# Performance work log

Hardware: AMD Instinct MI355X
Metric: run time of the kernel (lower is better)

Reference implementation:

```python
import jax, jax.numpy as jnp
import numpy as np

B, T, E, V, U = 4096, 80, 100, 10000, 1024


def setup_inputs() -> dict:
    key = jax.random.key(0)
    ks = jax.random.split(key, 8)
    def w(k, shape, fan_in):
        return jax.random.normal(k, shape, jnp.float32) * (1.0 / np.sqrt(fan_in))
    return {
        "inputs": jax.random.randint(ks[0], (B, T), 0, V, dtype=jnp.int32),
        "emb_table": w(ks[1], (V, E), E),
        "Wx0": w(ks[2], (E, U), E),
        "Wh0": w(ks[3], (U, U), U),
        "b0": jnp.zeros((U,), jnp.float32),
        "Wx1": w(ks[4], (U, U), U),
        "Wh1": w(ks[5], (U, U), U),
        "b1": jnp.zeros((U,), jnp.float32),
        "Wfc": w(ks[6], (U, 1), U),
        "bfc": jnp.zeros((1,), jnp.float32),
    }


def reference(inputs, emb_table, Wx0, Wh0, b0, Wx1, Wh1, b1, Wfc, bfc):
    # Embedding lookup: [B, T, E]
    x = emb_table[inputs]
    # Time-major for scan: [T, B, E]
    xs = jnp.swapaxes(x, 0, 1)
    h0_init = jnp.zeros((inputs.shape[0], Wh0.shape[0]), x.dtype)
    h1_init = jnp.zeros((inputs.shape[0], Wh1.shape[0]), x.dtype)

    def step(carry, xt):
        h0, h1 = carry
        # SimpleRNNCell: h' = tanh(x @ Wx + h @ Wh + b); output == new state
        h0 = jnp.tanh(xt @ Wx0 + h0 @ Wh0 + b0)
        h1 = jnp.tanh(h0 @ Wx1 + h1 @ Wh1 + b1)
        return (h0, h1), None

    (h0, h1), _ = jax.lax.scan(step, (h0_init, h1_init), xs)
    # Final dense + sigmoid on last layer-1 output
    prob = jax.nn.sigmoid(h1 @ Wfc + bfc)
    return prob
```

## Files before the change

kernel.cpp:

```cpp
#include <hip/hip_runtime.h>
#include <stdint.h>

#define B_ 4096
#define T_ 80
#define E_ 100
#define V_ 10000
#define U_ 1024

typedef unsigned short u16;
typedef __attribute__((ext_vector_type(8))) __bf16 bf16x8;
typedef __attribute__((ext_vector_type(4))) float f32x4;

__device__ __forceinline__ float bf2f(u16 u) {
    union { unsigned int i; float f; } v; v.i = ((unsigned int)u) << 16; return v.f;
}
__device__ __forceinline__ u16 f2bf(float f) {
    union { float f; unsigned int i; } v; v.f = f;
    unsigned int x = v.i;
    return (u16)((x + 0x7fffu + ((x >> 16) & 1u)) >> 16);
}

__device__ __forceinline__ void load16(const void* g, void* l) {
    __builtin_amdgcn_global_load_lds(
        (__attribute__((address_space(1))) void*)(uintptr_t)g,
        (__attribute__((address_space(3))) void*)(uint32_t)(uintptr_t)l,
        16, 0, 0);
}

__global__ void transpose_pad(const float* __restrict__ src, u16* __restrict__ dst,
                              int K, int N, int Kp)
{
    __shared__ u16 tile[32][33];
    const int k0 = blockIdx.x * 32;
    const int n0 = blockIdx.y * 32;
    const int tx = threadIdx.x & 31;
    const int ty = threadIdx.x >> 5;
#pragma unroll
    for (int i = 0; i < 4; i++) {
        int k = k0 + ty + i * 8;
        tile[ty + i * 8][tx] = (k < K) ? f2bf(src[(size_t)k * N + (n0 + tx)]) : (u16)0;
    }
    __syncthreads();
#pragma unroll
    for (int i = 0; i < 4; i++) {
        int n = n0 + ty + i * 8;
        dst[(size_t)n * Kp + (k0 + tx)] = tile[tx][ty + i * 8];
    }
}

__global__ void embed_pad(const float* __restrict__ emb, u16* __restrict__ dst)
{
    int id = blockIdx.x * 256 + threadIdx.x;
    int v = id >> 7, k = id & 127;
    dst[id] = (k < E_) ? f2bf(emb[v * E_ + k]) : (u16)0;
}

__global__ void __launch_bounds__(256, 2)
rnn_phase(const u16* __restrict__ embP, const int* __restrict__ idx,
          const u16* __restrict__ Wx0T, const u16* __restrict__ Wh0T, const float* __restrict__ b0,
          const u16* __restrict__ Wx1T, const u16* __restrict__ Wh1T, const float* __restrict__ b1,
          const u16* __restrict__ h0r, u16* __restrict__ h0w,
          const u16* __restrict__ h1r, u16* __restrict__ h1w,
          int do0, int do1)
{
    const int linear = blockIdx.x;
    const int layer  = linear >> 8;
    if (layer ? !do1 : !do0) return;

    __shared__ u16 As[2][128 * 64];
    __shared__ u16 Bs[2][128 * 64];
    const int tid  = threadIdx.x;
    const int lane = tid & 63;
    const int wave = tid >> 6;
    const int wm = wave >> 1, wn = wave & 1;
    const int sub = linear & 255;
    const int m0 = (sub & 31) * 128;
    const int n0 = (sub >> 5) * 128;

    const u16 *A1, *W1, *A2, *W2; const float* bias; u16* C; int K1; bool gather;
    if (layer == 0) { A1 = embP; W1 = Wx0T; K1 = 128;  gather = true;  A2 = h0r; W2 = Wh0T; bias = b0; C = h0w; }
    else            { A1 = h0r;  W1 = Wx1T; K1 = 1024; gather = false; A2 = h1r; W2 = Wh1T; bias = b1; C = h1w; }
    const int KB1 = K1 >> 6;
    const int TOT = KB1 + (U_ >> 6);

    const int r8 = lane >> 3;
    const int c8 = lane & 7;

    int gv[4];
    if (gather) {
#pragma unroll
        for (int cc = 0; cc < 4; cc++)
            gv[cc] = idx[(size_t)(m0 + wave * 32 + cc * 8 + r8) * T_];
    }

    const f32x4 z = {0.f, 0.f, 0.f, 0.f};
    f32x4 acc[4][4];
#pragma unroll
    for (int i = 0; i < 4; i++)
#pragma unroll
        for (int j = 0; j < 4; j++) acc[i][j] = z;

    const int l15 = lane & 15, q = lane >> 4, l7 = lane & 7;
    int offA[2][4], offB[2][4];
#pragma unroll
    for (int kk = 0; kk < 2; kk++) {
#pragma unroll
        for (int f = 0; f < 4; f++) {
            const int rA = wm * 64 + f * 16 + l15;
            const int rB = wn * 64 + f * 16 + l15;
            offA[kk][f] = rA * 64 + (((kk * 4 + q) ^ l7) * 8);
            offB[kk][f] = rB * 64 + (((kk * 4 + q) ^ l7) * 8);
        }
    }

    auto stage = [&](int u, int p) {
        u16* Ad = As[p] + wave * 2048;
        u16* Bd = Bs[p] + wave * 2048;
        if (u < KB1) {
            const int k0 = u * 64;
#pragma unroll
            for (int cc = 0; cc < 4; cc++) {
                const int row = wave * 32 + cc * 8 + r8;
                const int scw = (c8 ^ (row & 7)) * 8;
                const u16* ap = gather ? A1 + (size_t)gv[cc] * 128 + k0 + scw
                                       : A1 + (size_t)(m0 + row) * K1 + k0 + scw;
                load16(ap, Ad + cc * 512);
                load16(W1 + (size_t)(n0 + row) * K1 + k0 + scw, Bd + cc * 512);
            }
        } else {
            const int k0 = (u - KB1) * 64;
#pragma unroll
            for (int cc = 0; cc < 4; cc++) {
                const int row = wave * 32 + cc * 8 + r8;
                const int scw = (c8 ^ (row & 7)) * 8;
                load16(A2 + (size_t)(m0 + row) * U_ + k0 + scw, Ad + cc * 512);
                load16(W2 + (size_t)(n0 + row) * U_ + k0 + scw, Bd + cc * 512);
            }
        }
    };

    stage(0, 0);

#pragma unroll 1
    for (int u = 0; u < TOT; ++u) {
        const int p = u & 1;
        __syncthreads();
        if (u + 1 < TOT) stage(u + 1, p ^ 1);
#pragma unroll
        for (int kk = 0; kk < 2; kk++) {
            bf16x8 a[4], b[4];
#pragma unroll
            for (int f = 0; f < 4; f++) {
                a[f] = *reinterpret_cast<const bf16x8*>(As[p] + offA[kk][f]);
                b[f] = *reinterpret_cast<const bf16x8*>(Bs[p] + offB[kk][f]);
            }
#pragma unroll
            for (int i = 0; i < 4; i++)
#pragma unroll
                for (int j = 0; j < 4; j++)
                    acc[i][j] = __builtin_amdgcn_mfma_f32_16x16x32_bf16(a[i], b[j], acc[i][j], 0, 0, 0);
        }
    }

#pragma unroll
    for (int j = 0; j < 4; j++) {
        const int col = n0 + wn * 64 + j * 16 + l15;
        const float bv = bias[col];
#pragma unroll
        for (int i = 0; i < 4; i++) {
#pragma unroll
            for (int r = 0; r < 4; r++) {
                const int row = m0 + wm * 64 + i * 16 + (q << 2) + r;
                float x = acc[i][j][r] + bv;
                x = fminf(15.f, fmaxf(-15.f, x));
                float e = __expf(2.f * x);
                C[(size_t)row * U_ + col] = f2bf((e - 1.f) / (e + 1.f));
            }
        }
    }
}

__global__ void final_dense(const u16* __restrict__ h1, const float* __restrict__ Wfc,
                            const float* __restrict__ bfc, float* __restrict__ out)
{
    const int lane = threadIdx.x & 63;
    const int wave = threadIdx.x >> 6;
    const int row = blockIdx.x * 4 + wave;
    const u16* hp = h1 + (size_t)row * U_ + lane * 16;
    const float* wp = Wfc + lane * 16;
    float s = 0.f;
#pragma unroll
    for (int i = 0; i < 16; i++) s += bf2f(hp[i]) * wp[i];
#pragma unroll
    for (int off = 32; off; off >>= 1) s += __shfl_down(s, off);
    if (lane == 0) {
        float x = s + bfc[0];
        out[row] = 1.f / (1.f + __expf(-x));
    }
}

extern "C" void kernel_launch(void* const* d_in, const int* in_sizes, int n_in,
                              void* d_out, int out_size, void* d_ws, size_t ws_size,
                              hipStream_t stream)
{
    const int*   inputs = (const int*)d_in[0];
    const float* emb    = (const float*)d_in[1];
    const float* Wx0    = (const float*)d_in[2];
    const float* Wh0    = (const float*)d_in[3];
    const float* b0     = (const float*)d_in[4];
    const float* Wx1    = (const float*)d_in[5];
    const float* Wh1    = (const float*)d_in[6];
    const float* b1     = (const float*)d_in[7];
    const float* Wfc    = (const float*)d_in[8];
    const float* bfc    = (const float*)d_in[9];

    char* ws = (char*)d_ws;
    const size_t MB = 1 << 20;
    u16* h0b[2] = { (u16*)(ws + 0 * MB), (u16*)(ws + 8 * MB) };
    u16* h1b[2] = { (u16*)(ws + 16 * MB), (u16*)(ws + 24 * MB) };
    u16* embP = (u16*)(ws + 32 * MB);
    u16* Wx0T = (u16*)(ws + 35 * MB);
    u16* Wh0T = (u16*)(ws + 36 * MB);
    u16* Wx1T = (u16*)(ws + 38 * MB);
    u16* Wh1T = (u16*)(ws + 40 * MB);

    hipMemsetAsync(h0b[1], 0, 8 * MB, stream);
    hipMemsetAsync(h1b[1], 0, 8 * MB, stream);

    embed_pad<<<V_ * 128 / 256, 256, 0, stream>>>(emb, embP);
    transpose_pad<<<dim3(128 / 32, U_ / 32), 256, 0, stream>>>(Wx0, Wx0T, E_, U_, 128);
    transpose_pad<<<dim3(U_ / 32, U_ / 32), 256, 0, stream>>>(Wh0, Wh0T, U_, U_, U_);
    transpose_pad<<<dim3(U_ / 32, U_ / 32), 256, 0, stream>>>(Wx1, Wx1T, U_, U_, U_);
    transpose_pad<<<dim3(U_ / 32, U_ / 32), 256, 0, stream>>>(Wh1, Wh1T, U_, U_, U_);

    for (int p = 0; p <= T_; ++p) {
        const int e = p & 1;
        rnn_phase<<<512, 256, 0, stream>>>(embP, inputs + p,
                                           Wx0T, Wh0T, b0, Wx1T, Wh1T, b1,
                                           h0b[e ^ 1], h0b[e], h1b[e], h1b[e ^ 1],
                                           (int)(p < T_), (int)(p >= 1));
    }
    final_dense<<<B_ / 4, 256, 0, stream>>>(h1b[1], Wfc, bfc, (float*)d_out);
}
```

Measured before the change: 2.762 ms.

## Split layer-1 GEMM into separate input and recurrent roles across phases

Layer 1's two GEMMs are split across pipeline phases. One role computes h0·Wx1 into an fp32 staging buffer. A later role computes h1·Wh1, adds the staged product and applies tanh. This gives three equal-sized roles of 768 blocks per launch instead of one layer-0 role of 18 k-blocks and one layer-1 role of 32 k-blocks, aiming to cut the long-block critical path. The cost is one extra launch, 1.5 waves of blocks per phase, and a 16 MB fp32 write and read per step.

```diff
diff --git a/kernel.cpp b/kernel.cpp
--- a/kernel.cpp
+++ b/kernel.cpp
@@ -61,11 +61,12 @@
           const u16* __restrict__ Wx1T, const u16* __restrict__ Wh1T, const float* __restrict__ b1,
           const u16* __restrict__ h0r, u16* __restrict__ h0w,
           const u16* __restrict__ h1r, u16* __restrict__ h1w,
-          int do0, int do1)
+          const float* __restrict__ x1r, float* __restrict__ x1w,
+          int do0, int doX, int do1)
 {
     const int linear = blockIdx.x;
-    const int layer  = linear >> 8;
-    if (layer ? !do1 : !do0) return;
+    const int role   = linear >> 8;
+    if ((role == 0 && !do0) || (role == 1 && !doX) || (role == 2 && !do1)) return;
 
     __shared__ u16 As[2][128 * 64];
     __shared__ u16 Bs[2][128 * 64];
@@ -77,9 +78,11 @@
     const int m0 = (sub & 31) * 128;
     const int n0 = (sub >> 5) * 128;
 
-    const u16 *A1, *W1, *A2, *W2; const float* bias; u16* C; int K1; bool gather;
-    if (layer == 0) { A1 = embP; W1 = Wx0T; K1 = 128;  gather = true;  A2 = h0r; W2 = Wh0T; bias = b0; C = h0w; }
-    else            { A1 = h0r;  W1 = Wx1T; K1 = 1024; gather = false; A2 = h1r; W2 = Wh1T; bias = b1; C = h1w; }
+    const u16 *A1 = nullptr, *W1 = nullptr, *A2, *W2;
+    int K1 = 0; bool gather = false;
+    if (role == 0)      { A1 = embP; W1 = Wx0T; K1 = 128; gather = true; A2 = h0r; W2 = Wh0T; }
+    else if (role == 1) { A2 = h0r; W2 = Wx1T; }
+    else                { A2 = h1r; W2 = Wh1T; }
     const int KB1 = K1 >> 6;
     const int TOT = KB1 + (U_ >> 6);
 
@@ -162,19 +165,37 @@
         }
     }
 
-#pragma unroll
-    for (int j = 0; j < 4; j++) {
-        const int col = n0 + wn * 64 + j * 16 + l15;
-        const float bv = bias[col];
-#pragma unroll
-        for (int i = 0; i < 4; i++) {
-#pragma unroll
-            for (int r = 0; r < 4; r++) {
-                const int row = m0 + wm * 64 + i * 16 + (q << 2) + r;
-                float x = acc[i][j][r] + bv;
-                x = fminf(15.f, fmaxf(-15.f, x));
-                float e = __expf(2.f * x);
-                C[(size_t)row * U_ + col] = f2bf((e - 1.f) / (e + 1.f));
+    if (role == 1) {
+#pragma unroll
+        for (int j = 0; j < 4; j++) {
+            const int col = n0 + wn * 64 + j * 16 + l15;
+#pragma unroll
+            for (int i = 0; i < 4; i++) {
+#pragma unroll
+                for (int r = 0; r < 4; r++) {
+                    const int row = m0 + wm * 64 + i * 16 + (q << 2) + r;
+                    x1w[(size_t)row * U_ + col] = acc[i][j][r];
+                }
+            }
+        }
+    } else {
+        const float* bias = (role == 0) ? b0 : b1;
+        u16* C = (role == 0) ? h0w : h1w;
+#pragma unroll
+        for (int j = 0; j < 4; j++) {
+            const int col = n0 + wn * 64 + j * 16 + l15;
+            const float bv = bias[col];
+#pragma unroll
+            for (int i = 0; i < 4; i++) {
+#pragma unroll
+                for (int r = 0; r < 4; r++) {
+                    const int row = m0 + wm * 64 + i * 16 + (q << 2) + r;
+                    float x = acc[i][j][r] + bv;
+                    if (role == 2) x += x1r[(size_t)row * U_ + col];
+                    x = fminf(15.f, fmaxf(-15.f, x));
+                    float e = __expf(2.f * x);
+                    C[(size_t)row * U_ + col] = f2bf((e - 1.f) / (e + 1.f));
+                }
             }
         }
     }
@@ -216,13 +237,14 @@
 
     char* ws = (char*)d_ws;
     const size_t MB = 1 << 20;
-    u16* h0b[2] = { (u16*)(ws + 0 * MB), (u16*)(ws + 8 * MB) };
-    u16* h1b[2] = { (u16*)(ws + 16 * MB), (u16*)(ws + 24 * MB) };
-    u16* embP = (u16*)(ws + 32 * MB);
-    u16* Wx0T = (u16*)(ws + 35 * MB);
-    u16* Wh0T = (u16*)(ws + 36 * MB);
-    u16* Wx1T = (u16*)(ws + 38 * MB);
-    u16* Wh1T = (u16*)(ws + 40 * MB);
+    u16*   h0b[2] = { (u16*)(ws + 0 * MB), (u16*)(ws + 8 * MB) };
+    u16*   h1b[2] = { (u16*)(ws + 16 * MB), (u16*)(ws + 24 * MB) };
+    u16*   embP = (u16*)(ws + 32 * MB);
+    u16*   Wx0T = (u16*)(ws + 35 * MB);
+    u16*   Wh0T = (u16*)(ws + 36 * MB);
+    u16*   Wx1T = (u16*)(ws + 38 * MB);
+    u16*   Wh1T = (u16*)(ws + 40 * MB);
+    float* x1b[2] = { (float*)(ws + 48 * MB), (float*)(ws + 64 * MB) };
 
     hipMemsetAsync(h0b[1], 0, 8 * MB, stream);
     hipMemsetAsync(h1b[1], 0, 8 * MB, stream);
@@ -233,12 +255,13 @@
     transpose_pad<<<dim3(U_ / 32, U_ / 32), 256, 0, stream>>>(Wx1, Wx1T, U_, U_, U_);
     transpose_pad<<<dim3(U_ / 32, U_ / 32), 256, 0, stream>>>(Wh1, Wh1T, U_, U_, U_);
 
-    for (int p = 0; p <= T_; ++p) {
-        const int e = p & 1;
-        rnn_phase<<<512, 256, 0, stream>>>(embP, inputs + p,
+    for (int d = 0; d <= T_ + 1; ++d) {
+        const int e = d & 1;
+        rnn_phase<<<768, 256, 0, stream>>>(embP, inputs + d,
                                            Wx0T, Wh0T, b0, Wx1T, Wh1T, b1,
-                                           h0b[e ^ 1], h0b[e], h1b[e], h1b[e ^ 1],
-                                           (int)(p < T_), (int)(p >= 1));
+                                           h0b[e ^ 1], h0b[e], h1b[e ^ 1], h1b[e],
+                                           x1b[e ^ 1], x1b[e],
+                                           (int)(d < T_), (int)(d >= 1 && d <= T_), (int)(d >= 2));
     }
     final_dense<<<B_ / 4, 256, 0, stream>>>(h1b[1], Wfc, bfc, (float*)d_out);
 }
```

Result: slower. 3.960 ms (+43.4%).

## Load B weight fragments directly into registers, bypassing LDS, with a register double buffer

Applied to the files above, without the earlier changes.

Weight (B) tiles are no longer staged through shared memory. Each wave reads its MFMA B fragments straight from global memory into registers, double-buffered across iterations, while A still goes through LDS. The main loop is unrolled by two to alternate between the LDS buffers and the register buffers. This removes LDS traffic and LDS space for B. In exchange, the two waves that share a column block both fetch the same weight data, the global reads are strided and less coalesced, and more VGPRs are needed.

```diff
diff --git a/kernel.cpp b/kernel.cpp
--- a/kernel.cpp
+++ b/kernel.cpp
@@ -68,7 +68,6 @@
     if (layer ? !do1 : !do0) return;
 
     __shared__ u16 As[2][128 * 64];
-    __shared__ u16 Bs[2][128 * 64];
     const int tid  = threadIdx.x;
     const int lane = tid & 63;
     const int wave = tid >> 6;
@@ -101,21 +100,28 @@
         for (int j = 0; j < 4; j++) acc[i][j] = z;
 
     const int l15 = lane & 15, q = lane >> 4, l7 = lane & 7;
-    int offA[2][4], offB[2][4];
+
+    int offA[2][4];
 #pragma unroll
     for (int kk = 0; kk < 2; kk++) {
 #pragma unroll
         for (int f = 0; f < 4; f++) {
             const int rA = wm * 64 + f * 16 + l15;
-            const int rB = wn * 64 + f * 16 + l15;
             offA[kk][f] = rA * 64 + (((kk * 4 + q) ^ l7) * 8);
-            offB[kk][f] = rB * 64 + (((kk * 4 + q) ^ l7) * 8);
-        }
-    }
-
-    auto stage = [&](int u, int p) {
+        }
+    }
+
+    const u16* pB1[4];
+    const u16* pB2[4];
+#pragma unroll
+    for (int f = 0; f < 4; f++) {
+        const int rowB = n0 + wn * 64 + f * 16 + l15;
+        pB1[f] = W1 + (size_t)rowB * K1 + q * 8;
+        pB2[f] = W2 + (size_t)rowB * U_ + q * 8;
+    }
+
+    auto stageA = [&](int u, int p) {
         u16* Ad = As[p] + wave * 2048;
-        u16* Bd = Bs[p] + wave * 2048;
         if (u < KB1) {
             const int k0 = u * 64;
 #pragma unroll
@@ -125,7 +131,6 @@
                 const u16* ap = gather ? A1 + (size_t)gv[cc] * 128 + k0 + scw
                                        : A1 + (size_t)(m0 + row) * K1 + k0 + scw;
                 load16(ap, Ad + cc * 512);
-                load16(W1 + (size_t)(n0 + row) * K1 + k0 + scw, Bd + cc * 512);
             }
         } else {
             const int k0 = (u - KB1) * 64;
@@ -134,32 +139,56 @@
                 const int row = wave * 32 + cc * 8 + r8;
                 const int scw = (c8 ^ (row & 7)) * 8;
                 load16(A2 + (size_t)(m0 + row) * U_ + k0 + scw, Ad + cc * 512);
-                load16(W2 + (size_t)(n0 + row) * U_ + k0 + scw, Bd + cc * 512);
             }
         }
     };
 
-    stage(0, 0);
+    auto loadB = [&](int u, bf16x8 (&b)[8]) {
+        if (u < KB1) {
+            const int k0 = u * 64;
+#pragma unroll
+            for (int f = 0; f < 4; f++) {
+                b[f]     = *reinterpret_cast<const bf16x8*>(pB1[f] + k0);
+                b[4 + f] = *reinterpret_cast<const bf16x8*>(pB1[f] + k0 + 32);
+            }
+        } else {
+            const int k0 = (u - KB1) * 64;
+#pragma unroll
+            for (int f = 0; f < 4; f++) {
+                b[f]     = *reinterpret_cast<const bf16x8*>(pB2[f] + k0);
+                b[4 + f] = *reinterpret_cast<const bf16x8*>(pB2[f] + k0 + 32);
+            }
+        }
+    };
+
+    auto compute = [&](int p, const bf16x8 (&b)[8]) {
+#pragma unroll
+        for (int kk = 0; kk < 2; kk++) {
+            bf16x8 a[4];
+#pragma unroll
+            for (int f = 0; f < 4; f++)
+                a[f] = *reinterpret_cast<const bf16x8*>(As[p] + offA[kk][f]);
+#pragma unroll
+            for (int i = 0; i < 4; i++)
+#pragma unroll
+                for (int j = 0; j < 4; j++)
+                    acc[i][j] = __builtin_amdgcn_mfma_f32_16x16x32_bf16(a[i], b[kk * 4 + j], acc[i][j], 0, 0, 0);
+        }
+    };
+
+    bf16x8 bA[8], bB[8];
+    loadB(0, bA);
+    stageA(0, 0);
 
 #pragma unroll 1
-    for (int u = 0; u < TOT; ++u) {
-        const int p = u & 1;
+    for (int u = 0; u < TOT; u += 2) {
         __syncthreads();
-        if (u + 1 < TOT) stage(u + 1, p ^ 1);
-#pragma unroll
-        for (int kk = 0; kk < 2; kk++) {
-            bf16x8 a[4], b[4];
-#pragma unroll
-            for (int f = 0; f < 4; f++) {
-                a[f] = *reinterpret_cast<const bf16x8*>(As[p] + offA[kk][f]);
-                b[f] = *reinterpret_cast<const bf16x8*>(Bs[p] + offB[kk][f]);
-            }
-#pragma unroll
-            for (int i = 0; i < 4; i++)
-#pragma unroll
-                for (int j = 0; j < 4; j++)
-                    acc[i][j] = __builtin_amdgcn_mfma_f32_16x16x32_bf16(a[i], b[j], acc[i][j], 0, 0, 0);
-        }
+        stageA(u + 1, 1);
+        loadB(u + 1, bB);
+        compute(0, bA);
+        __syncthreads();
+        if (u + 2 < TOT) { stageA(u + 2, 0); loadB(u + 2, bA); }
+        compute(1, bB);
     }
 
 #pragma unroll
```

Measured after the change: 5.365 ms. 94.2% more time.
